# Performance work log

Hardware: AMD Instinct MI355X
Metric: run time of the kernel (lower is better)

The kernel has to match this reference:

```python
import jax, jax.numpy as jnp
import numpy as np

B, T, D, H, K, V = 2, 2048, 2048, 16, 128, 128


def _causal_conv(x, w):
    # x: [B,T,H,C], w: [H,C,4] -> depthwise causal conv, kernel size 4
    t = x.shape[1]
    xp = jnp.pad(x, ((0, 0), (3, 0), (0, 0), (0, 0)))
    return sum(xp[:, i:i + t] * w[:, :, i] for i in range(4))


def _l2norm(x):
    return x / jnp.maximum(jnp.linalg.norm(x, axis=-1, keepdims=True), 1e-12)


def _kda_scan(q, k, v, g, beta):
    # q,k: [B,T,H,K]; v: [B,T,H,V]; g: [B,T,H,K]; beta: [B,T,H]
    b, t, h, kd = q.shape
    vd = v.shape[-1]

    def step(S, inp):
        qt, kt, vt, gt, bt = inp
        S = S * jnp.exp(gt)[..., None]                       # per-key-channel decay
        err = vt - jnp.einsum('bhk,bhkv->bhv', kt, S)        # delta-rule error
        S = S + bt[..., None, None] * (kt[..., :, None] * err[..., None, :])
        ot = jnp.einsum('bhk,bhkv->bhv', qt, S)
        return S, ot

    tm = lambda a: jnp.moveaxis(a, 1, 0)
    S0 = jnp.zeros((b, h, kd, vd), q.dtype)
    _, ys = jax.lax.scan(step, S0, (tm(q), tm(k), tm(v), tm(g), tm(beta)))
    return jnp.moveaxis(ys, 0, 1)


def setup_inputs() -> dict:
    key = jax.random.key(0)
    ks = jax.random.split(key, 16)
    s = 0.02
    rng = np.random.default_rng(0)
    dt = np.exp(rng.uniform(size=H * K) * (np.log(0.1) - np.log(0.001)) + np.log(0.001)).clip(min=1e-4)
    dt_bias = (dt + np.log(-np.expm1(-dt))).astype(np.float32)
    A_log = np.log(rng.uniform(1.0, 16.0, size=H)).astype(np.float32)
    return {
        'x': jax.random.normal(ks[0], (B, T, D), jnp.float32),
        'Wq': jax.random.normal(ks[1], (H * K, D), jnp.float32) * s,
        'Wk': jax.random.normal(ks[2], (H * K, D), jnp.float32) * s,
        'Wv': jax.random.normal(ks[3], (H * V, D), jnp.float32) * s,
        'Wf1': jax.random.normal(ks[4], (V, D), jnp.float32) * s,
        'Wf2': jax.random.normal(ks[5], (H * K, V), jnp.float32) * s,
        'Wb': jax.random.normal(ks[6], (H, D), jnp.float32) * s,
        'Wg1': jax.random.normal(ks[7], (V, D), jnp.float32) * s,
        'Wg2': jax.random.normal(ks[8], (H * V, V), jnp.float32) * s,
        'bg': jnp.zeros((H * V,), jnp.float32),
        'o_norm_w': jnp.ones((V,), jnp.float32),
        'Wout': jax.random.normal(ks[9], (D, H * V), jnp.float32) * s,
        'A_log': jnp.asarray(A_log),
        'dt_bias': jnp.asarray(dt_bias),
        'qcw': jax.random.normal(ks[10], (H, K, 4), jnp.float32) * 0.1,
        'kcw': jax.random.normal(ks[11], (H, K, 4), jnp.float32) * 0.1,
        'vcw': jax.random.normal(ks[12], (H, V, 4), jnp.float32) * 0.1,
    }


def reference(x, Wq, Wk, Wv, Wf1, Wf2, Wb, Wg1, Wg2, bg, o_norm_w, Wout, A_log, dt_bias, qcw, kcw, vcw):
    b, t, d = x.shape
    h, kd = qcw.shape[0], qcw.shape[1]
    vd = vcw.shape[1]
    q = (x @ Wq.T).reshape(b, t, h, kd)
    k = (x @ Wk.T).reshape(b, t, h, kd)
    v = (x @ Wv.T).reshape(b, t, h, vd)
    q = _l2norm(jax.nn.silu(_causal_conv(q, qcw)))
    k = _l2norm(jax.nn.silu(_causal_conv(k, kcw)))
    v = jax.nn.silu(_causal_conv(v, vcw))
    g_raw = ((x @ Wf1.T) @ Wf2.T).reshape(b, t, h, kd)
    g = -jnp.exp(A_log)[None, None, :, None] * jax.nn.softplus(g_raw + dt_bias.reshape(h, kd))
    beta = jax.nn.sigmoid(x @ Wb.T)  # [B,T,H]
    y = _kda_scan(q, k, v, g, beta)  # [B,T,H,V]
    gate = ((x @ Wg1.T) @ Wg2.T + bg).reshape(b, t, h, vd)
    eps = 1.1920929e-07  # torch.finfo(float32).eps (F.rms_norm default)
    y = y * jax.lax.rsqrt(jnp.mean(y * y, axis=-1, keepdims=True) + eps) * o_norm_w
    y = y * jax.nn.sigmoid(gate)
    return y.reshape(b, t, h * vd) @ Wout.T
```

## Files before the change

### kernel.cpp

```cpp
#include <hip/hip_runtime.h>

typedef unsigned short u16;
typedef unsigned int u32;

using short8 = __attribute__((ext_vector_type(8))) short;
using s4     = __attribute__((ext_vector_type(4))) short;
using f32x4  = __attribute__((ext_vector_type(4))) float;

constexpr int kB = 2, kT = 2048, kD = 2048, kH = 16, kK = 128, kV = 128;
constexpr int kM  = kB * kT;
constexpr int kHK = kH * kK;
constexpr int kHV = kH * kV;
constexpr int CC  = 16;
constexpr int NCH = kT / CC;

constexpr size_t OFF_XB    = 0;
constexpr size_t OFF_WQKV  = 16777216;
constexpr size_t OFF_QC    = 0;
constexpr size_t OFF_YF    = 0;
constexpr size_t OFF_WF1B  = 41943040;
constexpr size_t OFF_WG1B  = 42467328;
constexpr size_t OFF_WBP   = 42991616;
constexpr size_t OFF_WF2B  = 43515904;
constexpr size_t OFF_WG2B  = 44040192;
constexpr size_t OFF_FGB   = 44564480;
constexpr size_t OFF_QKVR  = 48758784;
constexpr size_t OFF_QHB   = 48758784;
constexpr size_t OFF_KBB   = 65536000;
constexpr size_t OFF_KHB   = 82313216;
constexpr size_t OFF_YGB   = 82313216;
constexpr size_t OFF_GRAW  = 99090432;
constexpr size_t OFF_LAM   = 99090432;
constexpr size_t OFF_WINV  = 101187584;
constexpr size_t OFF_MM    = 105381888;
constexpr size_t OFF_GATEB = 115867648;
constexpr size_t OFF_WOUTB = 132644864;
constexpr size_t OFF_KC    = 141033472;
constexpr size_t OFF_VT    = 174587904;
constexpr size_t OFF_GK    = 208142336;
constexpr size_t OFF_BETA  = 241696768;

__device__ __forceinline__ u16 f2bf(float f) {
  union { float f; u32 u; } a; a.f = f;
  u32 u = a.u;
  u += 0x7fffu + ((u >> 16) & 1u);
  return (u16)(u >> 16);
}
__device__ __forceinline__ float bflo(u32 u) {
  union { u32 u; float f; } a; a.u = u << 16; return a.f;
}
__device__ __forceinline__ float bfhi(u32 u) {
  union { u32 u; float f; } a; a.u = u & 0xffff0000u; return a.f;
}
union BU { uint2 u; s4 s; };
__device__ __forceinline__ s4 us(uint2 u) { BU x; x.u = u; return x.s; }
__device__ __forceinline__ float sigmoidf(float x) {
  return __builtin_amdgcn_rcpf(1.0f + __expf(-x));
}
__device__ __forceinline__ f32x4 mfma16b(s4 a, s4 b, f32x4 c) {
  return __builtin_amdgcn_mfma_f32_16x16x16bf16_1k(a, b, c, 0, 0, 0);
}
__device__ __forceinline__ void packhl(const f32x4& v, uint2& hw, uint2& lw) {
  u16 h0 = f2bf(v[0]), h1 = f2bf(v[1]), h2 = f2bf(v[2]), h3 = f2bf(v[3]);
  hw.x = (u32)h0 | ((u32)h1 << 16); hw.y = (u32)h2 | ((u32)h3 << 16);
  lw.x = (u32)f2bf(v[0] - bflo(h0)) | ((u32)f2bf(v[1] - bflo(h1)) << 16);
  lw.y = (u32)f2bf(v[2] - bflo(h2)) | ((u32)f2bf(v[3] - bflo(h3)) << 16);
}

#define GL_AS1 __attribute__((address_space(1)))
#define GL_AS3 __attribute__((address_space(3)))
__device__ __forceinline__ void async_lds16(const void* g, void* l) {
  __builtin_amdgcn_global_load_lds((GL_AS1 u32*)(size_t)g,
                                   (GL_AS3 u32*)(u32)(size_t)l, 16, 0, 0);
}

__global__ __launch_bounds__(256) void cast_all(
    const float* __restrict__ x, const float* __restrict__ Wq,
    const float* __restrict__ Wk, const float* __restrict__ Wv,
    const float* __restrict__ Wout, const float* __restrict__ Wf1,
    const float* __restrict__ Wg1, const float* __restrict__ Wf2,
    const float* __restrict__ Wg2,
    u16* __restrict__ xb, u16* __restrict__ wqkv, u16* __restrict__ woutb,
    u16* __restrict__ wf1b, u16* __restrict__ wg1b, u16* __restrict__ wf2b,
    u16* __restrict__ wg2b) {
  long qi = (long)blockIdx.x * 256 + threadIdx.x;
  const float* src; u16* dst; long off;
  if (qi < 2097152)      { src = x;    dst = xb;             off = qi; }
  else if (qi < 3145728) { src = Wq;   dst = wqkv;           off = qi - 2097152; }
  else if (qi < 4194304) { src = Wk;   dst = wqkv + 4194304; off = qi - 3145728; }
  else if (qi < 5242880) { src = Wv;   dst = wqkv + 8388608; off = qi - 4194304; }
  else if (qi < 6291456) { src = Wout; dst = woutb;          off = qi - 5242880; }
  else if (qi < 6356992) { src = Wf1;  dst = wf1b;           off = qi - 6291456; }
  else if (qi < 6422528) { src = Wg1;  dst = wg1b;           off = qi - 6356992; }
  else if (qi < 6488064) { src = Wf2;  dst = wf2b;           off = qi - 6422528; }
  else                   { src = Wg2;  dst = wg2b;           off = qi - 6488064; }
  long i = off * 4;
  float4 v = *(const float4*)(src + i);
  uint2 st;
  st.x = (u32)f2bf(v.x) | ((u32)f2bf(v.y) << 16);
  st.y = (u32)f2bf(v.z) | ((u32)f2bf(v.w) << 16);
  *(uint2*)(dst + i) = st;
}

__global__ __launch_bounds__(256) void pad_wb(const float* __restrict__ Wb,
                                              u16* __restrict__ out) {
  int i = (blockIdx.x * 256 + threadIdx.x) * 4;
  int row = i >> 11;
  uint2 st; st.x = 0; st.y = 0;
  if (row < 16) {
    float4 v = *(const float4*)(Wb + i);
    st.x = (u32)f2bf(v.x) | ((u32)f2bf(v.y) << 16);
    st.y = (u32)f2bf(v.z) | ((u32)f2bf(v.w) << 16);
  }
  *(uint2*)(out + i) = st;
}

template <bool BF16OUT>
__global__ __launch_bounds__(256) void gemm_bt(const u16* __restrict__ A,
                                               const u16* __restrict__ B,
                                               void* __restrict__ Cout,
                                               int lda, int ldb, int ldc, int K) {
  __shared__ u16 As[128 * 32];
  __shared__ u16 Bs[128 * 32];
  const int tid  = threadIdx.x;
  const int lane = tid & 63;
  const int wave = tid >> 6;
  const int wm = (wave >> 1) * 64;
  const int wn = (wave & 1) * 64;
  const long row0 = (long)blockIdx.x * 128;
  const long col0 = (long)blockIdx.y * 128;
  const int srow = tid >> 2;
  const int scol = (tid & 3) * 8;
  const u16* aptr = A + (row0 + srow) * (size_t)lda + scol;
  const u16* bptr = B + (col0 + srow) * (size_t)ldb + scol;
  u16* asd  = &As[tid * 8];
  u16* asd2 = &As[2048 + tid * 8];
  u16* bsd  = &Bs[tid * 8];
  u16* bsd2 = &Bs[2048 + tid * 8];
  const int mrow = lane & 15;
  const int kq = (lane >> 4) * 8;
  f32x4 acc[4][4] = {};
  for (int k0 = 0; k0 < K; k0 += 32) {
    async_lds16(aptr, asd);
    async_lds16(aptr + (size_t)64 * lda, asd2);
    async_lds16(bptr, bsd);
    async_lds16(bptr + (size_t)64 * ldb, bsd2);
    aptr += 32; bptr += 32;
    __syncthreads();
    short8 af[4], bfr[4];
#pragma unroll
    for (int i = 0; i < 4; ++i)
      af[i] = *(const short8*)(&As[(wm + i * 16 + mrow) * 32 + kq]);
#pragma unroll
    for (int j = 0; j < 4; ++j)
      bfr[j] = *(const short8*)(&Bs[(wn + j * 16 + mrow) * 32 + kq]);
#pragma unroll
    for (int i = 0; i < 4; ++i)
#pragma unroll
      for (int j = 0; j < 4; ++j)
        acc[i][j] = __builtin_amdgcn_mfma_f32_16x16x32_bf16(af[i], bfr[j], acc[i][j], 0, 0, 0);
    __syncthreads();
  }
  const int cn = lane & 15;
  const int rq = (lane >> 4) * 4;
#pragma unroll
  for (int i = 0; i < 4; ++i)
#pragma unroll
    for (int j = 0; j < 4; ++j) {
      size_t r = (size_t)(row0 + wm + i * 16 + rq);
      size_t c = (size_t)(col0 + wn + j * 16 + cn);
#pragma unroll
      for (int rr = 0; rr < 4; ++rr) {
        if constexpr (BF16OUT)
          ((u16*)Cout)[(r + rr) * ldc + c] = f2bf(acc[i][j][rr]);
        else
          ((float*)Cout)[(r + rr) * ldc + c] = acc[i][j][rr];
      }
    }
}

__global__ __launch_bounds__(256) void convprep(
    const u16* __restrict__ qkv, const u16* __restrict__ graw,
    const u16* __restrict__ fgb,
    const float* __restrict__ qcw, const float* __restrict__ kcw,
    const float* __restrict__ vcw, const float* __restrict__ A_log,
    const float* __restrict__ dt_bias,
    float* __restrict__ qc, float* __restrict__ kc, float* __restrict__ vt,
    float* __restrict__ gdec, float* __restrict__ beta) {
  const int wid = blockIdx.x * 8 + (threadIdx.x >> 5);
  const int l32 = threadIdx.x & 31;
  const int h  = wid & 15;
  const int bt = wid >> 4;
  const int t  = bt & (kT - 1);
  const int b  = bt >> 11;
  const int c0 = l32 * 4;
  const size_t colofs = (size_t)h * kK + c0;
  const size_t rowb = (size_t)bt * 6144 + colofs;
  float wqt[4][4], wkt[4][4], wvt[4][4];
#pragma unroll
  for (int j = 0; j < 4; ++j) {
    *(float4*)wqt[j] = *(const float4*)(qcw + (colofs + j) * 4);
    *(float4*)wkt[j] = *(const float4*)(kcw + (colofs + j) * 4);
    *(float4*)wvt[j] = *(const float4*)(vcw + (colofs + j) * 4);
  }
  float qa[4] = {0.f, 0.f, 0.f, 0.f};
  float ka[4] = {0.f, 0.f, 0.f, 0.f};
  float va[4] = {0.f, 0.f, 0.f, 0.f};
#pragma unroll
  for (int i = 0; i < 4; ++i) {
    int tt = t - 3 + i;
    if (tt >= 0) {
      size_t ro = rowb - (size_t)(3 - i) * 6144;
      uint2 uq = *(const uint2*)(qkv + ro);
      uint2 uk = *(const uint2*)(qkv + ro + 2048);
      uint2 uv = *(const uint2*)(qkv + ro + 4096);
      float q0 = bflo(uq.x), q1 = bfhi(uq.x), q2 = bflo(uq.y), q3 = bfhi(uq.y);
      float k0 = bflo(uk.x), k1 = bfhi(uk.x), k2 = bflo(uk.y), k3 = bfhi(uk.y);
      float v0 = bflo(uv.x), v1 = bfhi(uv.x), v2 = bflo(uv.y), v3 = bfhi(uv.y);
      qa[0] = fmaf(q0, wqt[0][i], qa[0]); qa[1] = fmaf(q1, wqt[1][i], qa[1]);
      qa[2] = fmaf(q2, wqt[2][i], qa[2]); qa[3] = fmaf(q3, wqt[3][i], qa[3]);
      ka[0] = fmaf(k0, wkt[0][i], ka[0]); ka[1] = fmaf(k1, wkt[1][i], ka[1]);
      ka[2] = fmaf(k2, wkt[2][i], ka[2]); ka[3] = fmaf(k3, wkt[3][i], ka[3]);
      va[0] = fmaf(v0, wvt[0][i], va[0]); va[1] = fmaf(v1, wvt[1][i], va[1]);
      va[2] = fmaf(v2, wvt[2][i], va[2]); va[3] = fmaf(v3, wvt[3][i], va[3]);
    }
  }
  float sq = 0.f, sk = 0.f;
#pragma unroll
  for (int j = 0; j < 4; ++j) {
    qa[j] *= sigmoidf(qa[j]);
    ka[j] *= sigmoidf(ka[j]);
    va[j] *= sigmoidf(va[j]);
    sq = fmaf(qa[j], qa[j], sq);
    sk = fmaf(ka[j], ka[j], sk);
  }
#pragma unroll
  for (int m = 1; m < 32; m <<= 1) {
    sq += __shfl_xor(sq, m);
    sk += __shfl_xor(sk, m);
  }
  float qinv = __builtin_amdgcn_rcpf(fmaxf(__builtin_amdgcn_sqrtf(sq), 1e-12f));
  float kinv = __builtin_amdgcn_rcpf(fmaxf(__builtin_amdgcn_sqrtf(sk), 1e-12f));
  const int bh = b * kH + h;
  const size_t outb = ((size_t)bh * kT + t) * kK + c0;
  *(float4*)(qc + outb) =
      make_float4(qa[0] * qinv, qa[1] * qinv, qa[2] * qinv, qa[3] * qinv);
  *(float4*)(kc + outb) =
      make_float4(ka[0] * kinv, ka[1] * kinv, ka[2] * kinv, ka[3] * kinv);
  const size_t vtb = ((size_t)(bh * 8 + (c0 >> 4)) * kT + t) * 16 + (c0 & 15);
  *(float4*)(vt + vtb) = make_float4(va[0], va[1], va[2], va[3]);
  uint2 ug = *(const uint2*)(graw + (size_t)bt * kHK + colofs);
  float Ae = __expf(A_log[h]);
  float4 db = *(const float4*)(dt_bias + colofs);
  float g0 = bflo(ug.x) + db.x;
  float g1 = bfhi(ug.x) + db.y;
  float g2 = bflo(ug.y) + db.z;
  float g3 = bfhi(ug.y) + db.w;
  float sp0 = (g0 > 15.f) ? g0 : __logf(1.f + __expf(g0));
  float sp1 = (g1 > 15.f) ? g1 : __logf(1.f + __expf(g1));
  float sp2 = (g2 > 15.f) ? g2 : __logf(1.f + __expf(g2));
  float sp3 = (g3 > 15.f) ? g3 : __logf(1.f + __expf(g3));
  *(float4*)(gdec + outb) = make_float4(-Ae * sp0, -Ae * sp1, -Ae * sp2, -Ae * sp3);
  if (l32 == 0) {
    float bv = bflo((u32)fgb[(size_t)bt * 384 + 256 + h]);
    beta[(size_t)bh * kT + t] = sigmoidf(bv);
  }
}

__global__ __launch_bounds__(256) void kda_p1(
    const float* __restrict__ qc, const float* __restrict__ kc,
    const float* __restrict__ gk, const float* __restrict__ betap,
    u16* __restrict__ qhb, u16* __restrict__ khb, u16* __restrict__ kbt,
    float* __restrict__ lamC, u16* __restrict__ whv, u16* __restrict__ wlv,
    u16* __restrict__ mhv, u16* __restrict__ mlv) {
  __shared__ float kL[CC][132], qL[CC][132], gL[CC][132];
  __shared__ float As[CC][CC], Ms[CC][CC];
  __shared__ float bet[CC];
  const int tid = threadIdx.x;
  const int bh = blockIdx.x >> 7;
  const int ch = blockIdx.x & 127;
  const size_t base = ((size_t)bh * kT + ch * CC) * kK;
  const int e = tid * 8;
  const int t = e >> 7, k = e & 127;
  {
    *(float4*)&kL[t][k]     = *(const float4*)(kc + base + e);
    *(float4*)&kL[t][k + 4] = *(const float4*)(kc + base + e + 4);
    *(float4*)&qL[t][k]     = *(const float4*)(qc + base + e);
    *(float4*)&qL[t][k + 4] = *(const float4*)(qc + base + e + 4);
    *(float4*)&gL[t][k]     = *(const float4*)(gk + base + e);
    *(float4*)&gL[t][k + 4] = *(const float4*)(gk + base + e + 4);
    if (tid < CC) bet[tid] = betap[(size_t)bh * kT + ch * CC + tid];
  }
  __syncthreads();
  if (tid < kK) {
    float a = gL[0][tid];
#pragma unroll
    for (int tt = 1; tt < CC; ++tt) { a += gL[tt][tid]; gL[tt][tid] = a; }
  }
  __syncthreads();
  float khr[8], qhr[8], kbw[8];
  u16 kbv[8];
  u32 pk[4] = {0,0,0,0}, pq[4] = {0,0,0,0};
#pragma unroll
  for (int j = 0; j < 8; ++j) {
    float G  = gL[t][k + j];
    float GC = gL[CC - 1][k + j];
    float eg = __expf(G);
    float kh = kL[t][k + j] * eg;
    float qh = qL[t][k + j] * eg;
    float kb = kL[t][k + j] * __expf(GC - G);
    u16 a = f2bf(kh), b_ = f2bf(qh), c = f2bf(kb);
    pk[j >> 1] |= ((u32)a)  << (16 * (j & 1));
    pq[j >> 1] |= ((u32)b_) << (16 * (j & 1));
    kbv[j] = c;
    khr[j] = bflo((u32)a);
    qhr[j] = bflo((u32)b_);
    kbw[j] = bflo((u32)c) * __expf(-GC);
  }
  *(uint4*)(khb + base + e) = *(uint4*)pk;
  *(uint4*)(qhb + base + e) = *(uint4*)pq;
  {
    const size_t kb2 = ((size_t)bh * NCH + ch) * (size_t)(kK * CC) +
                       (size_t)k * CC + t;
#pragma unroll
    for (int j = 0; j < 8; ++j) kbt[kb2 + (size_t)j * CC] = kbv[j];
  }
  if (tid < kK)
    lamC[((size_t)bh * NCH + ch) * kK + tid] = __expf(gL[CC - 1][tid]);
  __syncthreads();
#pragma unroll
  for (int j = 0; j < 8; ++j) {
    kL[t][k + j] = khr[j];
    qL[t][k + j] = qhr[j];
    gL[t][k + j] = kbw[j];
  }
  __syncthreads();
  {
    const int t2 = tid >> 4, s = tid & 15;
    float av = 0.f, mv = 0.f;
    for (int kk = 0; kk < kK; ++kk) {
      float w = gL[s][kk];
      av = fmaf(kL[t2][kk], w, av);
      mv = fmaf(qL[t2][kk], w, mv);
    }
    As[t2][s] = (s < t2)  ? av : 0.f;
    Ms[t2][s] = (s <= t2) ? mv : 0.f;
  }
  __syncthreads();
  const size_t smb = ((size_t)bh * NCH + ch) * 256;
  if (tid < CC) {
    const int s = tid;
    float x[CC];
#pragma unroll
    for (int tt = 0; tt < CC; ++tt) {
      float sum = 0.f;
      for (int r = 0; r < tt; ++r) sum += As[tt][r] * x[r];
      x[tt] = ((tt == s) ? bet[tt] : 0.f) - bet[tt] * sum;
    }
#pragma unroll
    for (int tt = 0; tt < CC; ++tt) {
      u16 xh = f2bf(x[tt]);
      whv[smb + tt * 16 + s] = xh;
      wlv[smb + tt * 16 + s] = f2bf(x[tt] - bflo((u32)xh));
    }
  }
  {
    float mvv = Ms[tid >> 4][tid & 15];
    u16 mhh = f2bf(mvv);
    mhv[smb + tid] = mhh;
    mlv[smb + tid] = f2bf(mvv - bflo((u32)mhh));
  }
}

__global__ __launch_bounds__(64, 1) void kda_p2(
    const u16* __restrict__ khb, const u16* __restrict__ qhb,
    const u16* __restrict__ kbt, const float* __restrict__ lamC,
    const u16* __restrict__ whg, const u16* __restrict__ wlg,
    const u16* __restrict__ mhg, const u16* __restrict__ mlg,
    const float* __restrict__ vt, float* __restrict__ yf) {
  const int lane = threadIdx.x;
  const int m15 = lane & 15, q = lane >> 4;
  const int blk = blockIdx.x;
  const int bh = blk & 31, vs = blk >> 5;
  const u16*  khp  = khb + (size_t)bh * (kT * kK) + (size_t)m15 * kK + 4 * q;
  const u16*  qhp  = qhb + (size_t)bh * (kT * kK) + (size_t)m15 * kK + 4 * q;
  const u16*  kbp  = kbt + (size_t)bh * (NCH * kK * CC) + (size_t)m15 * CC + 4 * q;
  const float* lamp = lamC + (size_t)bh * (NCH * kK) + 4 * q;
  const size_t smb  = (size_t)bh * (NCH * 256) + (size_t)m15 * 16 + 4 * q;
  const float* vp  = vt + ((size_t)(bh * 8 + vs) * kT + 4 * q) * 16 + m15;
  float*       yp  = yf + ((size_t)bh * kT + 4 * q) * kV + vs * 16 + m15;

  f32x4 S[8] = {};
  uint2 Sh[8] = {}, Sl[8] = {};

  uint2 khA[8], qhA[8]; float vA[4];
  uint2 khB2[8], qhB2[8]; float vB[4];

#define LKQ(KH, QH, VV, ch) {                                                  \
    const u16* k_ = khp + (size_t)(ch) * (CC * kK);                            \
    const u16* q_ = qhp + (size_t)(ch) * (CC * kK);                            \
    _Pragma("unroll") for (int j = 0; j < 8; ++j) {                            \
      KH[j] = *(const uint2*)(k_ + 16 * j);                                    \
      QH[j] = *(const uint2*)(q_ + 16 * j);                                    \
    }                                                                          \
    const float* v_ = vp + (size_t)(ch) * (CC * 16);                           \
    _Pragma("unroll") for (int r = 0; r < 4; ++r) VV[r] = v_[16 * r];          \
  }

#define CHUNK(KH, QH, VV, KH2, QH2, VV2, ch) {                                 \
            \
    uint2 kb_[8]; float4 lam_[8];                                              \
    const u16* kb0 = kbp + (size_t)(ch) * (kK * CC);                           \
    _Pragma("unroll") for (int j = 0; j < 8; ++j)                              \
      kb_[j] = *(const uint2*)(kb0 + 16 * j * CC);                             \
    const float* l0 = lamp + (size_t)(ch) * kK;                                \
    _Pragma("unroll") for (int j = 0; j < 8; ++j)                              \
      lam_[j] = *(const float4*)(l0 + 16 * j);                                 \
    uint2 wh_ = *(const uint2*)(whg + smb + (size_t)(ch) * 256);               \
    uint2 wl_ = *(const uint2*)(wlg + smb + (size_t)(ch) * 256);               \
    uint2 mh_ = *(const uint2*)(mhg + smb + (size_t)(ch) * 256);               \
    uint2 ml_ = *(const uint2*)(mlg + smb + (size_t)(ch) * 256);               \
           \
    f32x4 z_ = {0.f, 0.f, 0.f, 0.f};                                           \
    f32x4 P0 = z_, P1 = z_, Q0 = z_, Q1 = z_;                                  \
    _Pragma("unroll") for (int j = 0; j < 4; ++j) {                            \
      P0 = mfma16b(us(KH[j]), us(Sl[j]), P0);                                  \
      P0 = mfma16b(us(KH[j]), us(Sh[j]), P0);                                  \
      P1 = mfma16b(us(KH[j + 4]), us(Sl[j + 4]), P1);                          \
      P1 = mfma16b(us(KH[j + 4]), us(Sh[j + 4]), P1);                          \
      Q0 = mfma16b(us(QH[j]), us(Sl[j]), Q0);                                  \
      Q0 = mfma16b(us(QH[j]), us(Sh[j]), Q0);                                  \
      Q1 = mfma16b(us(QH[j + 4]), us(Sl[j + 4]), Q1);                          \
      Q1 = mfma16b(us(QH[j + 4]), us(Sh[j + 4]), Q1);                          \
    }                                                                          \
                                        \
    if ((ch) + 1 < NCH) LKQ(KH2, QH2, VV2, (ch) + 1);                          \
                    \
    f32x4 T_, Qt_;                                                             \
    _Pragma("unroll") for (int r = 0; r < 4; ++r) {                            \
      T_[r]  = VV[r] - (P0[r] + P1[r]);                                        \
      Qt_[r] = Q0[r] + Q1[r];                                                  \
    }                                                                          \
    uint2 Thw, Tlw; packhl(T_, Thw, Tlw);                                      \
                                                              \
    f32x4 U_ = mfma16b(us(wh_), us(Thw), z_);                                  \
    U_ = mfma16b(us(wh_), us(Tlw), U_);                                        \
    U_ = mfma16b(us(wl_), us(Thw), U_);                                        \
    uint2 Uhw, Ulw; packhl(U_, Uhw, Ulw);                                      \
                                                   \
    f32x4 O_ = mfma16b(us(mh_), us(Uhw), Qt_);                                 \
    O_ = mfma16b(us(mh_), us(Ulw), O_);                                        \
    O_ = mfma16b(us(ml_), us(Uhw), O_);                                        \
    {                                                                          \
      float* y_ = yp + (size_t)(ch) * (CC * kV);                               \
      _Pragma("unroll") for (int r = 0; r < 4; ++r) y_[r * kV] = O_[r];        \
    }                                                                          \
      \
    _Pragma("unroll") for (int j = 0; j < 8; ++j) {                            \
      f32x4 Sv = S[j];                                                         \
      _Pragma("unroll") for (int r = 0; r < 4; ++r) Sv[r] *= lam_[j][r];       \
      Sv = mfma16b(us(kb_[j]), us(Ulw), Sv);                                   \
      Sv = mfma16b(us(kb_[j]), us(Uhw), Sv);                                   \
      S[j] = Sv;                                                               \
      packhl(Sv, Sh[j], Sl[j]);                                                \
    }                                                                          \
  }

  LKQ(khA, qhA, vA, 0);
  for (int ch = 0; ch < NCH; ch += 2) {
    CHUNK(khA, qhA, vA, khB2, qhB2, vB, ch);
    CHUNK(khB2, qhB2, vB, khA, qhA, vA, ch + 1);
  }
#undef LKQ
#undef CHUNK
}

__global__ __launch_bounds__(256) void postk(
    const float* __restrict__ yf, const u16* __restrict__ gateb,
    const float* __restrict__ bg, const float* __restrict__ onw,
    u16* __restrict__ ygb) {
  const int wid  = blockIdx.x * 4 + (threadIdx.x >> 6);
  const int lane = threadIdx.x & 63;
  const int h  = wid & 15;
  const int bt = wid >> 4;
  const int t  = bt & (kT - 1);
  const int b  = bt >> 11;
  const int v0 = lane * 2;
  const size_t yi = ((size_t)(b * kH + h) * kT + t) * kV + v0;
  float2 yv = *(const float2*)(yf + yi);
  float s = yv.x * yv.x + yv.y * yv.y;
#pragma unroll
  for (int m = 1; m < 64; m <<= 1) s += __shfl_xor(s, m);
  float scale = rsqrtf(s * (1.0f / 128.0f) + 1.1920929e-07f);
  const size_t gi = (size_t)bt * kHV + (size_t)h * kV + v0;
  u32 ug = *(const u32*)(gateb + gi);
  float g0 = bflo(ug) + bg[h * kV + v0];
  float g1 = bfhi(ug) + bg[h * kV + v0 + 1];
  float r0 = yv.x * scale * onw[v0] * sigmoidf(g0);
  float r1 = yv.y * scale * onw[v0 + 1] * sigmoidf(g1);
  *(u32*)(ygb + gi) = (u32)f2bf(r0) | ((u32)f2bf(r1) << 16);
}

extern "C" void kernel_launch(void* const* d_in, const int* in_sizes, int n_in,
                              void* d_out, int out_size, void* d_ws, size_t ws_size,
                              hipStream_t stream) {
  (void)in_sizes; (void)n_in; (void)out_size; (void)ws_size;
  const float* x    = (const float*)d_in[0];
  const float* Wq   = (const float*)d_in[1];
  const float* Wk   = (const float*)d_in[2];
  const float* Wv   = (const float*)d_in[3];
  const float* Wf1  = (const float*)d_in[4];
  const float* Wf2  = (const float*)d_in[5];
  const float* Wb   = (const float*)d_in[6];
  const float* Wg1  = (const float*)d_in[7];
  const float* Wg2  = (const float*)d_in[8];
  const float* bg   = (const float*)d_in[9];
  const float* onw  = (const float*)d_in[10];
  const float* Wout = (const float*)d_in[11];
  const float* A_log   = (const float*)d_in[12];
  const float* dt_bias = (const float*)d_in[13];
  const float* qcw  = (const float*)d_in[14];
  const float* kcw  = (const float*)d_in[15];
  const float* vcw  = (const float*)d_in[16];

  char* ws = (char*)d_ws;
  u16* xb     = (u16*)(ws + OFF_XB);
  u16* wqkv   = (u16*)(ws + OFF_WQKV);
  u16* wf1b   = (u16*)(ws + OFF_WF1B);
  u16* wg1b   = (u16*)(ws + OFF_WG1B);
  u16* wbp    = (u16*)(ws + OFF_WBP);
  u16* wf2b   = (u16*)(ws + OFF_WF2B);
  u16* wg2b   = (u16*)(ws + OFF_WG2B);
  u16* woutb  = (u16*)(ws + OFF_WOUTB);
  u16* fgb    = (u16*)(ws + OFF_FGB);
  u16* qkvraw = (u16*)(ws + OFF_QKVR);
  u16* graw   = (u16*)(ws + OFF_GRAW);
  u16* gateb  = (u16*)(ws + OFF_GATEB);
  u16* qhb    = (u16*)(ws + OFF_QHB);
  u16* khb    = (u16*)(ws + OFF_KHB);
  u16* kbb    = (u16*)(ws + OFF_KBB);
  u16* ygb    = (u16*)(ws + OFF_YGB);
  u16* whv    = (u16*)(ws + OFF_WINV);
  u16* wlv    = (u16*)(ws + OFF_WINV + 2097152);
  u16* mhv    = (u16*)(ws + OFF_MM);
  u16* mlv    = (u16*)(ws + OFF_MM + 2097152);
  float* qcf   = (float*)(ws + OFF_QC);
  float* kcf   = (float*)(ws + OFF_KC);
  float* vtf   = (float*)(ws + OFF_VT);
  float* gkf   = (float*)(ws + OFF_GK);
  float* betaf = (float*)(ws + OFF_BETA);
  float* yff   = (float*)(ws + OFF_YF);
  float* lamf  = (float*)(ws + OFF_LAM);

  cast_all<<<25600, 256, 0, stream>>>(x, Wq, Wk, Wv, Wout, Wf1, Wg1, Wf2, Wg2,
                                      xb, wqkv, woutb, wf1b, wg1b, wf2b, wg2b);
  pad_wb<<<(128 * 2048 / 4 + 255) / 256, 256, 0, stream>>>(Wb, wbp);

  dim3 blk(256);
  gemm_bt<true><<<dim3(kM / 128, 6144 / 128), blk, 0, stream>>>(
      xb, wqkv, qkvraw, kD, kD, 6144, kD);
  gemm_bt<true><<<dim3(kM / 128, 384 / 128), blk, 0, stream>>>(
      xb, wf1b, fgb, kD, kD, 384, kD);
  gemm_bt<true><<<dim3(kM / 128, kHK / 128), blk, 0, stream>>>(
      fgb, wf2b, graw, 384, kV, kHK, kV);
  gemm_bt<true><<<dim3(kM / 128, kHV / 128), blk, 0, stream>>>(
      fgb + 128, wg2b, gateb, 384, kV, kHV, kV);

  convprep<<<kB * kT * kH / 8, 256, 0, stream>>>(qkvraw, graw, fgb,
                                                 qcw, kcw, vcw, A_log, dt_bias,
                                                 qcf, kcf, vtf, gkf, betaf);

  kda_p1<<<32 * NCH, 256, 0, stream>>>(qcf, kcf, gkf, betaf,
                                       qhb, khb, kbb, lamf,
                                       whv, wlv, mhv, mlv);
  kda_p2<<<256, 64, 0, stream>>>(khb, qhb, kbb, lamf,
                                 whv, wlv, mhv, mlv, vtf, yff);

  postk<<<kB * kT * kH / 4, 256, 0, stream>>>(yff, gateb, bg, onw, ygb);

  gemm_bt<false><<<dim3(kM / 128, kD / 128), blk, 0, stream>>>(
      ygb, woutb, (float*)d_out, kHV, kHV, kD, kHV);
}
```

Baseline: 783.8 us.

## Share per-chunk K/Q/W/M tiles via LDS across four waves in scan kernel

The recurrent scan kernel now runs 4 waves per block, each owning a 16-wide slice of V, and the block cooperatively stages each chunk's k, q, k-beta, W, M, lambda and v tiles into double-buffered shared memory. Before, each single-wave block fetched these tiles from global memory on its own. Loads for the next chunk are issued into registers before the current chunk's compute and written to LDS afterwards. The MFMA accumulation chains are also split into independent hi/lo partial sums to shorten dependency chains. In exchange, the grid drops from 256 to 64 blocks, each chunk step adds a __syncthreads, and reads now go through LDS.

```diff
diff --git a/kernel.cpp b/kernel.cpp
--- a/kernel.cpp
+++ b/kernel.cpp
@@ -372,107 +372,129 @@
   }
 }
 
-__global__ __launch_bounds__(64, 1) void kda_p2(
+__global__ __launch_bounds__(256, 1) void kda_p2(
     const u16* __restrict__ khb, const u16* __restrict__ qhb,
     const u16* __restrict__ kbt, const float* __restrict__ lamC,
     const u16* __restrict__ whg, const u16* __restrict__ wlg,
     const u16* __restrict__ mhg, const u16* __restrict__ mlg,
     const float* __restrict__ vt, float* __restrict__ yf) {
-  const int lane = threadIdx.x;
+  __shared__ u16 khs[2][CC][136];
+  __shared__ u16 qhs[2][CC][136];
+  __shared__ u16 kbs[2][kK][20];
+  __shared__ float vsx[2][CC][68];
+  __shared__ u16 whs[2][CC][20], wls[2][CC][20];
+  __shared__ u16 mhs[2][CC][20], mls[2][CC][20];
+  __shared__ float lamx[2][kK];
+  const int tid = threadIdx.x;
+  const int w = tid >> 6, lane = tid & 63;
   const int m15 = lane & 15, q = lane >> 4;
   const int blk = blockIdx.x;
-  const int bh = blk & 31, vs = blk >> 5;
-  const u16*  khp  = khb + (size_t)bh * (kT * kK) + (size_t)m15 * kK + 4 * q;
-  const u16*  qhp  = qhb + (size_t)bh * (kT * kK) + (size_t)m15 * kK + 4 * q;
-  const u16*  kbp  = kbt + (size_t)bh * (NCH * kK * CC) + (size_t)m15 * CC + 4 * q;
-  const float* lamp = lamC + (size_t)bh * (NCH * kK) + 4 * q;
-  const size_t smb  = (size_t)bh * (NCH * 256) + (size_t)m15 * 16 + 4 * q;
-  const float* vp  = vt + ((size_t)(bh * 8 + vs) * kT + 4 * q) * 16 + m15;
-  float*       yp  = yf + ((size_t)bh * kT + 4 * q) * kV + vs * 16 + m15;
+  const int bh = blk & 31, g = blk >> 5;
+  const size_t khbase = (size_t)bh * (kT * kK);
+  const size_t kbbase = (size_t)bh * (NCH * (kK * CC));
+  const size_t smbase = (size_t)bh * (NCH * 256);
+  const int tv = (tid & 63) >> 2, c4 = (tid & 3) * 4;
 
   f32x4 S[8] = {};
   uint2 Sh[8] = {}, Sl[8] = {};
 
-  uint2 khA[8], qhA[8]; float vA[4];
-  uint2 khB2[8], qhB2[8]; float vB[4];
-
-#define LKQ(KH, QH, VV, ch) {                                                  \
-    const u16* k_ = khp + (size_t)(ch) * (CC * kK);                            \
-    const u16* q_ = qhp + (size_t)(ch) * (CC * kK);                            \
-    _Pragma("unroll") for (int j = 0; j < 8; ++j) {                            \
-      KH[j] = *(const uint2*)(k_ + 16 * j);                                    \
-      QH[j] = *(const uint2*)(q_ + 16 * j);                                    \
-    }                                                                          \
-    const float* v_ = vp + (size_t)(ch) * (CC * 16);                           \
-    _Pragma("unroll") for (int r = 0; r < 4; ++r) VV[r] = v_[16 * r];          \
-  }
-
-#define CHUNK(KH, QH, VV, KH2, QH2, VV2, ch) {                                 \
-            \
-    uint2 kb_[8]; float4 lam_[8];                                              \
-    const u16* kb0 = kbp + (size_t)(ch) * (kK * CC);                           \
-    _Pragma("unroll") for (int j = 0; j < 8; ++j)                              \
-      kb_[j] = *(const uint2*)(kb0 + 16 * j * CC);                             \
-    const float* l0 = lamp + (size_t)(ch) * kK;                                \
-    _Pragma("unroll") for (int j = 0; j < 8; ++j)                              \
-      lam_[j] = *(const float4*)(l0 + 16 * j);                                 \
-    uint2 wh_ = *(const uint2*)(whg + smb + (size_t)(ch) * 256);               \
-    uint2 wl_ = *(const uint2*)(wlg + smb + (size_t)(ch) * 256);               \
-    uint2 mh_ = *(const uint2*)(mhg + smb + (size_t)(ch) * 256);               \
-    uint2 ml_ = *(const uint2*)(mlg + smb + (size_t)(ch) * 256);               \
-           \
-    f32x4 z_ = {0.f, 0.f, 0.f, 0.f};                                           \
-    f32x4 P0 = z_, P1 = z_, Q0 = z_, Q1 = z_;                                  \
-    _Pragma("unroll") for (int j = 0; j < 4; ++j) {                            \
-      P0 = mfma16b(us(KH[j]), us(Sl[j]), P0);                                  \
-      P0 = mfma16b(us(KH[j]), us(Sh[j]), P0);                                  \
-      P1 = mfma16b(us(KH[j + 4]), us(Sl[j + 4]), P1);                          \
-      P1 = mfma16b(us(KH[j + 4]), us(Sh[j + 4]), P1);                          \
-      Q0 = mfma16b(us(QH[j]), us(Sl[j]), Q0);                                  \
-      Q0 = mfma16b(us(QH[j]), us(Sh[j]), Q0);                                  \
-      Q1 = mfma16b(us(QH[j + 4]), us(Sl[j + 4]), Q1);                          \
-      Q1 = mfma16b(us(QH[j + 4]), us(Sh[j + 4]), Q1);                          \
-    }                                                                          \
-                                        \
-    if ((ch) + 1 < NCH) LKQ(KH2, QH2, VV2, (ch) + 1);                          \
-                    \
-    f32x4 T_, Qt_;                                                             \
-    _Pragma("unroll") for (int r = 0; r < 4; ++r) {                            \
-      T_[r]  = VV[r] - (P0[r] + P1[r]);                                        \
-      Qt_[r] = Q0[r] + Q1[r];                                                  \
-    }                                                                          \
-    uint2 Thw, Tlw; packhl(T_, Thw, Tlw);                                      \
-                                                              \
-    f32x4 U_ = mfma16b(us(wh_), us(Thw), z_);                                  \
-    U_ = mfma16b(us(wh_), us(Tlw), U_);                                        \
-    U_ = mfma16b(us(wl_), us(Thw), U_);                                        \
-    uint2 Uhw, Ulw; packhl(U_, Uhw, Ulw);                                      \
-                                                   \
-    f32x4 O_ = mfma16b(us(mh_), us(Uhw), Qt_);                                 \
-    O_ = mfma16b(us(mh_), us(Ulw), O_);                                        \
-    O_ = mfma16b(us(ml_), us(Uhw), O_);                                        \
-    {                                                                          \
-      float* y_ = yp + (size_t)(ch) * (CC * kV);                               \
-      _Pragma("unroll") for (int r = 0; r < 4; ++r) y_[r * kV] = O_[r];        \
-    }                                                                          \
-      \
-    _Pragma("unroll") for (int j = 0; j < 8; ++j) {                            \
-      f32x4 Sv = S[j];                                                         \
-      _Pragma("unroll") for (int r = 0; r < 4; ++r) Sv[r] *= lam_[j][r];       \
-      Sv = mfma16b(us(kb_[j]), us(Ulw), Sv);                                   \
-      Sv = mfma16b(us(kb_[j]), us(Uhw), Sv);                                   \
-      S[j] = Sv;                                                               \
-      packhl(Sv, Sh[j], Sl[j]);                                                \
-    }                                                                          \
-  }
-
-  LKQ(khA, qhA, vA, 0);
-  for (int ch = 0; ch < NCH; ch += 2) {
-    CHUNK(khA, qhA, vA, khB2, qhB2, vB, ch);
-    CHUNK(khB2, qhB2, vB, khA, qhA, vA, ch + 1);
-  }
-#undef LKQ
-#undef CHUNK
+  uint4 rkh, rqh, rkb; float4 rv; u32 rw, rl2, rm, rml; float rlam;
+  auto loadR = [&](int ch) {
+    const size_t cb = khbase + (size_t)ch * (CC * kK) + tid * 8;
+    rkh = *(const uint4*)(khb + cb);
+    rqh = *(const uint4*)(qhb + cb);
+    rkb = *(const uint4*)(kbt + kbbase + (size_t)ch * (kK * CC) + tid * 8);
+    rv  = *(const float4*)(vt +
+          ((size_t)(bh * 8 + g * 4 + w) * kT + ch * CC + tv) * 16 + c4);
+    if (tid < 128) {
+      const size_t sm = smbase + (size_t)ch * 256;
+      rw  = *(const u32*)(whg + sm + tid * 2);
+      rl2 = *(const u32*)(wlg + sm + tid * 2);
+      rm  = *(const u32*)(mhg + sm + tid * 2);
+      rml = *(const u32*)(mlg + sm + tid * 2);
+      rlam = lamC[(size_t)bh * (NCH * kK) + (size_t)ch * kK + tid];
+    }
+  };
+  auto writeS = [&](int b) {
+    const int tr = tid >> 4, tc = (tid & 15) * 8;
+    *(uint4*)&khs[b][tr][tc] = rkh;
+    *(uint4*)&qhs[b][tr][tc] = rqh;
+    u16* kd = &kbs[b][tid >> 1][(tid & 1) * 8];
+    *(uint2*)kd = make_uint2(rkb.x, rkb.y);
+    *(uint2*)(kd + 4) = make_uint2(rkb.z, rkb.w);
+    *(float4*)&vsx[b][tv][w * 16 + c4] = rv;
+    if (tid < 128) {
+      const int wr = tid >> 3, wc = (tid & 7) * 2;
+      *(u32*)&whs[b][wr][wc] = rw;
+      *(u32*)&wls[b][wr][wc] = rl2;
+      *(u32*)&mhs[b][wr][wc] = rm;
+      *(u32*)&mls[b][wr][wc] = rml;
+      lamx[b][tid] = rlam;
+    }
+  };
+
+  float* yp = yf + ((size_t)bh * kT + 4 * q) * kV + g * 64 + w * 16 + m15;
+
+  loadR(0);
+  writeS(0);
+  __syncthreads();
+  for (int ch = 0; ch < NCH; ++ch) {
+    const int b = ch & 1;
+    if (ch + 1 < NCH) loadR(ch + 1);
+    f32x4 z = {0.f, 0.f, 0.f, 0.f};
+    f32x4 Ph = z, Pl = z, Qh = z, Ql = z;
+#pragma unroll
+    for (int j = 0; j < 8; ++j) {
+      s4 aK = *(const s4*)&khs[b][m15][16 * j + 4 * q];
+      s4 aQ = *(const s4*)&qhs[b][m15][16 * j + 4 * q];
+      Ph = mfma16b(aK, us(Sh[j]), Ph);
+      Pl = mfma16b(aK, us(Sl[j]), Pl);
+      Qh = mfma16b(aQ, us(Sh[j]), Qh);
+      Ql = mfma16b(aQ, us(Sl[j]), Ql);
+    }
+    f32x4 T_, Qt;
+#pragma unroll
+    for (int r = 0; r < 4; ++r) {
+      float vv = vsx[b][4 * q + r][16 * w + m15];
+      T_[r] = vv - (Ph[r] + Pl[r]);
+      Qt[r] = Qh[r] + Ql[r];
+    }
+    uint2 Thw, Tlw; packhl(T_, Thw, Tlw);
+    s4 aWh = *(const s4*)&whs[b][m15][4 * q];
+    s4 aWl = *(const s4*)&wls[b][m15][4 * q];
+    f32x4 Ua = mfma16b(aWh, us(Thw), z);
+    f32x4 Ub = mfma16b(aWh, us(Tlw), z);
+    Ub = mfma16b(aWl, us(Thw), Ub);
+    f32x4 U_;
+#pragma unroll
+    for (int r = 0; r < 4; ++r) U_[r] = Ua[r] + Ub[r];
+    uint2 Uhw, Ulw; packhl(U_, Uhw, Ulw);
+    s4 aMh = *(const s4*)&mhs[b][m15][4 * q];
+    s4 aMl = *(const s4*)&mls[b][m15][4 * q];
+    f32x4 Oa = mfma16b(aMh, us(Uhw), Qt);
+    f32x4 Ob = mfma16b(aMh, us(Ulw), z);
+    Ob = mfma16b(aMl, us(Uhw), Ob);
+    {
+      float* y_ = yp + (size_t)ch * (CC * kV);
+#pragma unroll
+      for (int r = 0; r < 4; ++r) y_[r * kV] = Oa[r] + Ob[r];
+    }
+#pragma unroll
+    for (int j = 0; j < 8; ++j) {
+      s4 aB = *(const s4*)&kbs[b][16 * j + m15][4 * q];
+      f32x4 SLa = mfma16b(aB, us(Ulw), z);
+      f32x4 Sv = S[j];
+      float4 lm = *(const float4*)&lamx[b][16 * j + 4 * q];
+      Sv[0] *= lm.x; Sv[1] *= lm.y; Sv[2] *= lm.z; Sv[3] *= lm.w;
+      Sv = mfma16b(aB, us(Uhw), Sv);
+#pragma unroll
+      for (int r = 0; r < 4; ++r) Sv[r] += SLa[r];
+      S[j] = Sv;
+      packhl(Sv, Sh[j], Sl[j]);
+    }
+    if (ch + 1 < NCH) writeS(b ^ 1);
+    __syncthreads();
+  }
 }
 
 __global__ __launch_bounds__(256) void postk(
@@ -573,7 +595,7 @@
   kda_p1<<<32 * NCH, 256, 0, stream>>>(qcf, kcf, gkf, betaf,
                                        qhb, khb, kbb, lamf,
                                        whv, wlv, mhv, mlv);
-  kda_p2<<<256, 64, 0, stream>>>(khb, qhb, kbb, lamf,
+  kda_p2<<<64, 256, 0, stream>>>(khb, qhb, kbb, lamf,
                                  whv, wlv, mhv, mlv, vtf, yff);
 
   postk<<<kB * kT * kH / 4, 256, 0, stream>>>(yff, gateb, bg, onw, ygb);
```

Measured after the change: 774.2 us. About the same (-1.2%).
